# Performance work log

Hardware: AMD Instinct MI355X
Metric: run time of the kernel (lower is better)

The kernel has to match this reference:

```python
import jax, jax.numpy as jnp
import numpy as np

N_BOXES = 1_000_000
EPS = 1e-6


def box2corners(box):
    """(..., 5) [x,y,w,h,angle] -> (..., 4, 2) corners (mmcv box2corners)."""
    x, y, w, h, a = (box[..., i] for i in range(5))
    dx = jnp.asarray([0.5, -0.5, -0.5, 0.5], box.dtype) * w[..., None]  # (...,4)
    dy = jnp.asarray([0.5, 0.5, -0.5, -0.5], box.dtype) * h[..., None]
    cos, sin = jnp.cos(a)[..., None], jnp.sin(a)[..., None]
    cx = dx * cos - dy * sin + x[..., None]
    cy = dx * sin + dy * cos + y[..., None]
    return jnp.stack([cx, cy], axis=-1)


def box_intersection(c1, c2):
    """All 4x4 edge-pair segment intersections. c1,c2: (N,4,2).
    Returns pts (N,4,4,2), mask (N,4,4)."""
    roll = jnp.array([1, 2, 3, 0])
    line1 = jnp.concatenate([c1, c1[:, roll, :]], axis=-1)  # (N,4,4): x1,y1,x2,y2
    line2 = jnp.concatenate([c2, c2[:, roll, :]], axis=-1)
    l1 = line1[:, :, None, :]  # (N,4,1,4)
    l2 = line2[:, None, :, :]  # (N,1,4,4)
    x1, y1, x2, y2 = l1[..., 0], l1[..., 1], l1[..., 2], l1[..., 3]
    x3, y3, x4, y4 = l2[..., 0], l2[..., 1], l2[..., 2], l2[..., 3]
    num = (y4 - y3) * (x2 - x1) - (x4 - x3) * (y2 - y1)
    den_t = (x4 - x3) * (y1 - y3) - (y4 - y3) * (x1 - x3)
    safe = jnp.where(num == 0.0, 1.0, num)
    t = jnp.where(num == 0.0, -1.0, den_t / safe)
    mask_t = (t > 0) & (t < 1)
    den_u = (x2 - x1) * (y1 - y3) - (y2 - y1) * (x1 - x3)
    u = jnp.where(num == 0.0, -1.0, -den_u / safe)
    mask_u = (u > 0) & (u < 1)
    mask = mask_t & mask_u
    t2 = den_t / (num + 1e-8)
    pts = jnp.stack([x1 + t2 * (x2 - x1), y1 + t2 * (y2 - y1)], axis=-1)
    pts = pts * mask[..., None].astype(pts.dtype)
    return pts, mask


def box1_in_box2(c1, c2):
    """Which corners of c1 lie inside box c2. (N,4,2)x(N,4,2)->(N,4) bool."""
    a = c2[:, 0:1, :]
    b = c2[:, 1:2, :]
    d = c2[:, 3:4, :]
    ab, ad, am = b - a, d - a, c1 - a
    pab = jnp.sum(ab * am, -1) / jnp.sum(ab * ab, -1)
    pad_ = jnp.sum(ad * am, -1) / jnp.sum(ad * ad, -1)
    e = 1e-6
    return (pab > -e) & (pab < 1 + e) & (pad_ > -e) & (pad_ < 1 + e)


def intersection_area(c1, c2):
    """Differentiable rotated-box intersection area via convex polygon clipping."""
    inter_pts, inter_mask = box_intersection(c1, c2)
    m1 = box1_in_box2(c1, c2)
    m2 = box1_in_box2(c2, c1)
    n = c1.shape[0]
    verts = jnp.concatenate([c1, c2, inter_pts.reshape(n, 16, 2)], axis=1)  # (N,24,2)
    mask = jnp.concatenate([m1, m2, inter_mask.reshape(n, 16)], axis=1)     # (N,24)
    k = jnp.sum(mask, axis=-1)  # num valid vertices per box
    mf = mask.astype(verts.dtype)
    mean = jnp.sum(verts * mf[..., None], axis=1, keepdims=True) / \
        jnp.maximum(k, 1).astype(verts.dtype)[:, None, None]
    vn = verts - mean
    # sort valid vertices counterclockwise by angle around centroid; invalid last
    ang = jnp.where(mask, jnp.arctan2(vn[..., 1], vn[..., 0]), 1e9)
    order = jnp.argsort(ang, axis=-1)
    vs = jnp.take_along_axis(verts, order[..., None], axis=1)  # (N,24,2)
    idx = jnp.arange(24)
    nxt = jnp.where(idx[None, :] + 1 < k[:, None], idx[None, :] + 1, 0)
    v_next = jnp.take_along_axis(vs, nxt[..., None], axis=1)
    cross = vs[..., 0] * v_next[..., 1] - vs[..., 1] * v_next[..., 0]
    valid = idx[None, :] < k[:, None]
    return jnp.abs(jnp.sum(jnp.where(valid, cross, 0.0), axis=-1)) * 0.5


def fpdiou_loss(pred, target):
    c1 = box2corners(pred)
    c2 = box2corners(target)
    inter = intersection_area(c1, c2)
    area1 = pred[:, 2] * pred[:, 3]
    area2 = target[:, 2] * target[:, 3]
    iou = inter / (area1 + area2 - inter)
    iou = jnp.maximum(iou, EPS)
    # corner-distance term (detached in original via .detach().cpu().numpy())
    p = jax.lax.stop_gradient(c1)
    g = jax.lax.stop_gradient(c2)
    ps = jnp.take_along_axis(p, jnp.argsort(p[..., 0], axis=-1)[..., None], axis=1)
    gs = jnp.take_along_axis(g, jnp.argsort(g[..., 0], axis=-1)[..., None], axis=1)
    d = 2.0 * (gs[:, 0, 0] - ps[:, 0, 0]) ** 2 \
        + (ps[:, 1, 0] - gs[:, 1, 0]) ** 2 + (ps[:, 1, 1] - gs[:, 1, 1]) ** 2 \
        + (ps[:, 2, 0] - gs[:, 2, 0]) ** 2 + (ps[:, 2, 1] - gs[:, 2, 1]) ** 2 \
        + (ps[:, 3, 0] - gs[:, 3, 0]) ** 2 + (ps[:, 3, 1] - gs[:, 3, 1]) ** 2
    res = d / (4.0 * 1024.0 ** 2)
    loss = 1.0 - iou + res  # mode='linear'
    return jnp.mean(loss)   # reduction='mean', loss_weight=1.0


def setup_inputs() -> dict:
    key = jax.random.key(0)
    k1, k2, k3, k4 = jax.random.split(key, 4)
    xy = jax.random.uniform(k1, (N_BOXES, 2), minval=0.0, maxval=1024.0)
    wh = jax.random.uniform(k2, (N_BOXES, 2), minval=8.0, maxval=96.0)
    ang = jax.random.uniform(k3, (N_BOXES, 1), minval=-np.pi / 2, maxval=np.pi / 2)
    pred = jnp.concatenate([xy, wh, ang], axis=-1).astype(jnp.float32)
    scale = jnp.asarray([4.0, 4.0, 3.0, 3.0, 0.1], jnp.float32)
    target = pred + jax.random.normal(k4, (N_BOXES, 5), jnp.float32) * scale
    target = target.at[:, 2:4].set(jnp.maximum(target[:, 2:4], 4.0))
    return {"pred": pred, "target": target}


def reference(pred, target):
    return fpdiou_loss(pred, target)
```

## Files before the change

kernel.cpp:

```cpp
#include <hip/hip_runtime.h>

#define BS 128
#define NV 24

__device__ __forceinline__ void sort4_by_x(const float* x, const float* y,
                                           float* sx, float* sy) {
    int rk[4];
#pragma unroll
    for (int a = 0; a < 4; a++) {
        int r = 0;
#pragma unroll
        for (int b = 0; b < 4; b++) {
            r += (x[b] < x[a]) || (x[b] == x[a] && b < a);
        }
        rk[a] = r;
    }
#pragma unroll
    for (int r = 0; r < 4; r++) {
        float vx = 0.f, vy = 0.f;
#pragma unroll
        for (int a = 0; a < 4; a++) {
            if (rk[a] == r) { vx = x[a]; vy = y[a]; }
        }
        sx[r] = vx; sy[r] = vy;
    }
}

__global__ __launch_bounds__(BS, 2)
void fpdiou_kernel(const float* __restrict__ pred, const float* __restrict__ tgt,
                   float* __restrict__ partial, int n)
{
    __shared__ float s_vx[NV * BS];
    __shared__ float s_vy[NV * BS];
    __shared__ float s_ang[NV * BS];
    __shared__ float s_red[2];

    const int tid = threadIdx.x;
    const int i = blockIdx.x * BS + tid;
    float loss = 0.f;

    if (i < n) {
        const float* pp = pred + (size_t)i * 5;
        const float* gg = tgt  + (size_t)i * 5;
        const float pw = pp[2], ph = pp[3];
        const float gw = gg[2], gh = gg[3];

        float c1x[4], c1y[4], c2x[4], c2y[4];
        {
            const float DX[4] = {0.5f, -0.5f, -0.5f, 0.5f};
            const float DY[4] = {0.5f,  0.5f, -0.5f, -0.5f};
            float s, c;
            sincosf(pp[4], &s, &c);
            float x = pp[0], y = pp[1];
#pragma unroll
            for (int q = 0; q < 4; q++) {
                float dx = DX[q] * pw, dy = DY[q] * ph;
                c1x[q] = dx * c - dy * s + x;
                c1y[q] = dx * s + dy * c + y;
            }
            sincosf(gg[4], &s, &c);
            x = gg[0]; y = gg[1];
#pragma unroll
            for (int q = 0; q < 4; q++) {
                float dx = DX[q] * gw, dy = DY[q] * gh;
                c2x[q] = dx * c - dy * s + x;
                c2y[q] = dx * s + dy * c + y;
            }
        }

        int k = 0;
        {
            const float ax = c2x[0], ay = c2y[0];
            const float abx = c2x[1] - ax, aby = c2y[1] - ay;
            const float adx = c2x[3] - ax, ady = c2y[3] - ay;
            const float dab = abx * abx + aby * aby;
            const float dad = adx * adx + ady * ady;
#pragma unroll
            for (int q = 0; q < 4; q++) {
                float amx = c1x[q] - ax, amy = c1y[q] - ay;
                float pab = (abx * amx + aby * amy) / dab;
                float pd  = (adx * amx + ady * amy) / dad;
                const float e = 1e-6f;
                if (pab > -e && pab < 1.f + e && pd > -e && pd < 1.f + e) {
                    s_vx[k * BS + tid] = c1x[q];
                    s_vy[k * BS + tid] = c1y[q];
                    k++;
                }
            }
        }
        {
            const float ax = c1x[0], ay = c1y[0];
            const float abx = c1x[1] - ax, aby = c1y[1] - ay;
            const float adx = c1x[3] - ax, ady = c1y[3] - ay;
            const float dab = abx * abx + aby * aby;
            const float dad = adx * adx + ady * ady;
#pragma unroll
            for (int q = 0; q < 4; q++) {
                float amx = c2x[q] - ax, amy = c2y[q] - ay;
                float pab = (abx * amx + aby * amy) / dab;
                float pd  = (adx * amx + ady * amy) / dad;
                const float e = 1e-6f;
                if (pab > -e && pab < 1.f + e && pd > -e && pd < 1.f + e) {
                    s_vx[k * BS + tid] = c2x[q];
                    s_vy[k * BS + tid] = c2y[q];
                    k++;
                }
            }
        }
#pragma unroll
        for (int a = 0; a < 4; a++) {
            const float x1 = c1x[a], y1 = c1y[a];
            const float x2 = c1x[(a + 1) & 3], y2 = c1y[(a + 1) & 3];
            const float ex = x2 - x1, ey = y2 - y1;
#pragma unroll
            for (int b = 0; b < 4; b++) {
                const float x3 = c2x[b], y3 = c2y[b];
                const float x4 = c2x[(b + 1) & 3], y4 = c2y[(b + 1) & 3];
                const float fx = x4 - x3, fy = y4 - y3;
                const float num = fy * ex - fx * ey;
                if (num != 0.f) {
                    const float dx13 = x1 - x3, dy13 = y1 - y3;
                    const float den_t = fx * dy13 - fy * dx13;
                    const float t = den_t / num;
                    const float den_u = ex * dy13 - ey * dx13;
                    const float u = -den_u / num;
                    if (t > 0.f && t < 1.f && u > 0.f && u < 1.f) {
                        const float t2 = den_t / (num + 1e-8f);
                        s_vx[k * BS + tid] = x1 + t2 * ex;
                        s_vy[k * BS + tid] = y1 + t2 * ey;
                        k++;
                    }
                }
            }
        }

        float area = 0.f;
        if (k > 0) {
            float sx = 0.f, sy = 0.f;
            for (int v = 0; v < k; v++) {
                sx += s_vx[v * BS + tid];
                sy += s_vy[v * BS + tid];
            }
            const float mx = sx / (float)k;
            const float my = sy / (float)k;
            for (int v = 0; v < k; v++) {
                s_ang[v * BS + tid] =
                    atan2f(s_vy[v * BS + tid] - my, s_vx[v * BS + tid] - mx);
            }
            for (int v = 1; v < k; v++) {
                float a = s_ang[v * BS + tid];
                float x = s_vx[v * BS + tid];
                float y = s_vy[v * BS + tid];
                int j = v - 1;
                while (j >= 0 && s_ang[j * BS + tid] > a) {
                    s_ang[(j + 1) * BS + tid] = s_ang[j * BS + tid];
                    s_vx[(j + 1) * BS + tid] = s_vx[j * BS + tid];
                    s_vy[(j + 1) * BS + tid] = s_vy[j * BS + tid];
                    j--;
                }
                s_ang[(j + 1) * BS + tid] = a;
                s_vx[(j + 1) * BS + tid] = x;
                s_vy[(j + 1) * BS + tid] = y;
            }
            float cr = 0.f;
            for (int v = 0; v < k; v++) {
                int nx = (v + 1 < k) ? v + 1 : 0;
                cr += s_vx[v * BS + tid] * s_vy[nx * BS + tid]
                    - s_vy[v * BS + tid] * s_vx[nx * BS + tid];
            }
            area = fabsf(cr) * 0.5f;
        }

        const float a1 = pw * ph, a2 = gw * gh;
        float iou = area / (a1 + a2 - area);
        iou = fmaxf(iou, 1e-6f);

        float psx[4], psy[4], gsx[4], gsy[4];
        sort4_by_x(c1x, c1y, psx, psy);
        sort4_by_x(c2x, c2y, gsx, gsy);
        const float d0 = gsx[0] - psx[0];
        float d = 2.f * d0 * d0;
#pragma unroll
        for (int q = 1; q < 4; q++) {
            float dxq = psx[q] - gsx[q];
            float dyq = psy[q] - gsy[q];
            d += dxq * dxq + dyq * dyq;
        }
        const float res = d * (1.f / 4194304.f);

        loss = 1.f - iou + res;
    }

#pragma unroll
    for (int off = 32; off > 0; off >>= 1)
        loss += __shfl_down(loss, off, 64);
    if ((tid & 63) == 0) s_red[tid >> 6] = loss;
    __syncthreads();
    if (tid == 0) partial[blockIdx.x] = s_red[0] + s_red[1];
}

__global__ void fpdiou_reduce_kernel(const float* __restrict__ partial, int nblk,
                                     float* __restrict__ out, float inv_n)
{
    __shared__ float red[4];
    float s = 0.f;
    for (int i = threadIdx.x; i < nblk; i += blockDim.x)
        s += partial[i];
#pragma unroll
    for (int off = 32; off > 0; off >>= 1)
        s += __shfl_down(s, off, 64);
    if ((threadIdx.x & 63) == 0) red[threadIdx.x >> 6] = s;
    __syncthreads();
    if (threadIdx.x == 0) {
        float t = red[0] + red[1] + red[2] + red[3];
        out[0] = t * inv_n;
    }
}

extern "C" void kernel_launch(void* const* d_in, const int* in_sizes, int n_in,
                              void* d_out, int out_size, void* d_ws, size_t ws_size,
                              hipStream_t stream)
{
    const float* pred = (const float*)d_in[0];
    const float* tgt  = (const float*)d_in[1];
    float* out = (float*)d_out;
    const int n = in_sizes[0] / 5;
    const int nblk = (n + BS - 1) / BS;
    float* partial = (float*)d_ws;

    fpdiou_kernel<<<nblk, BS, 0, stream>>>(pred, tgt, partial, n);
    fpdiou_reduce_kernel<<<1, 256, 0, stream>>>(partial, nblk, out, 1.f / (float)n);
}
```

Baseline: 155.2 us.

## Replace atan2 sort with pseudo-angle successor search and single-wave blocks

Replaces atan2f plus insertion sort of polygon vertices with a cheap pseudo-angle and a per-vertex successor search that computes the shoelace area without sorting. Accumulates the centroid while vertices are collected, drops the num!=0 branch, caps vertex count at 16, and shrinks shared arrays. Uses 64-thread blocks so the block reduction needs no barrier, and widens the final reduce kernel to 1024 threads. The O(k^2) successor search and the unguarded division when num is zero (relying on NaN comparisons failing) change numerics slightly and add quadratic work for large k.

```diff
diff --git a/kernel.cpp b/kernel.cpp
--- a/kernel.cpp
+++ b/kernel.cpp
@@ -1,7 +1,7 @@
 #include <hip/hip_runtime.h>
 
-#define BS 128
-#define NV 24
+#define BS 64
+#define NVMAX 16
 
 __device__ __forceinline__ void sort4_by_x(const float* x, const float* y,
                                            float* sx, float* sy) {
@@ -24,16 +24,21 @@
         }
         sx[r] = vx; sy[r] = vy;
     }
+}
+
+__device__ __forceinline__ float pseudo_angle(float dx, float dy) {
+    float s = fabsf(dx) + fabsf(dy);
+    float r = (s == 0.f) ? 0.f : (1.f - dx / s);
+    return copysignf(r, dy);
 }
 
 __global__ __launch_bounds__(BS, 2)
 void fpdiou_kernel(const float* __restrict__ pred, const float* __restrict__ tgt,
                    float* __restrict__ partial, int n)
 {
-    __shared__ float s_vx[NV * BS];
-    __shared__ float s_vy[NV * BS];
-    __shared__ float s_ang[NV * BS];
-    __shared__ float s_red[2];
+    __shared__ float s_vx[NVMAX * BS];
+    __shared__ float s_vy[NVMAX * BS];
+    __shared__ float s_p [NVMAX * BS];
 
     const int tid = threadIdx.x;
     const int i = blockIdx.x * BS + tid;
@@ -69,6 +74,7 @@
         }
 
         int k = 0;
+        float sx = 0.f, sy = 0.f;
         {
             const float ax = c2x[0], ay = c2y[0];
             const float abx = c2x[1] - ax, aby = c2y[1] - ay;
@@ -84,6 +90,7 @@
                 if (pab > -e && pab < 1.f + e && pd > -e && pd < 1.f + e) {
                     s_vx[k * BS + tid] = c1x[q];
                     s_vy[k * BS + tid] = c1y[q];
+                    sx += c1x[q]; sy += c1y[q];
                     k++;
                 }
             }
@@ -103,6 +110,7 @@
                 if (pab > -e && pab < 1.f + e && pd > -e && pd < 1.f + e) {
                     s_vx[k * BS + tid] = c2x[q];
                     s_vy[k * BS + tid] = c2y[q];
+                    sx += c2x[q]; sy += c2y[q];
                     k++;
                 }
             }
@@ -110,63 +118,55 @@
 #pragma unroll
         for (int a = 0; a < 4; a++) {
             const float x1 = c1x[a], y1 = c1y[a];
-            const float x2 = c1x[(a + 1) & 3], y2 = c1y[(a + 1) & 3];
-            const float ex = x2 - x1, ey = y2 - y1;
+            const float ex = c1x[(a + 1) & 3] - x1, ey = c1y[(a + 1) & 3] - y1;
 #pragma unroll
             for (int b = 0; b < 4; b++) {
                 const float x3 = c2x[b], y3 = c2y[b];
-                const float x4 = c2x[(b + 1) & 3], y4 = c2y[(b + 1) & 3];
-                const float fx = x4 - x3, fy = y4 - y3;
+                const float fx = c2x[(b + 1) & 3] - x3, fy = c2y[(b + 1) & 3] - y3;
                 const float num = fy * ex - fx * ey;
-                if (num != 0.f) {
-                    const float dx13 = x1 - x3, dy13 = y1 - y3;
-                    const float den_t = fx * dy13 - fy * dx13;
-                    const float t = den_t / num;
-                    const float den_u = ex * dy13 - ey * dx13;
-                    const float u = -den_u / num;
-                    if (t > 0.f && t < 1.f && u > 0.f && u < 1.f) {
-                        const float t2 = den_t / (num + 1e-8f);
-                        s_vx[k * BS + tid] = x1 + t2 * ex;
-                        s_vy[k * BS + tid] = y1 + t2 * ey;
-                        k++;
-                    }
+                const float dx13 = x1 - x3, dy13 = y1 - y3;
+                const float den_t = fx * dy13 - fy * dx13;
+                const float den_u = ex * dy13 - ey * dx13;
+                const float t = den_t / num;
+                const float u = -den_u / num;
+                if (t > 0.f && t < 1.f && u > 0.f && u < 1.f && k < NVMAX) {
+                    const float t2 = den_t / (num + 1e-8f);
+                    const float ix = x1 + t2 * ex, iy = y1 + t2 * ey;
+                    s_vx[k * BS + tid] = ix;
+                    s_vy[k * BS + tid] = iy;
+                    sx += ix; sy += iy;
+                    k++;
                 }
             }
         }
 
         float area = 0.f;
         if (k > 0) {
-            float sx = 0.f, sy = 0.f;
-            for (int v = 0; v < k; v++) {
-                sx += s_vx[v * BS + tid];
-                sy += s_vy[v * BS + tid];
-            }
             const float mx = sx / (float)k;
             const float my = sy / (float)k;
             for (int v = 0; v < k; v++) {
-                s_ang[v * BS + tid] =
-                    atan2f(s_vy[v * BS + tid] - my, s_vx[v * BS + tid] - mx);
-            }
-            for (int v = 1; v < k; v++) {
-                float a = s_ang[v * BS + tid];
-                float x = s_vx[v * BS + tid];
-                float y = s_vy[v * BS + tid];
-                int j = v - 1;
-                while (j >= 0 && s_ang[j * BS + tid] > a) {
-                    s_ang[(j + 1) * BS + tid] = s_ang[j * BS + tid];
-                    s_vx[(j + 1) * BS + tid] = s_vx[j * BS + tid];
-                    s_vy[(j + 1) * BS + tid] = s_vy[j * BS + tid];
-                    j--;
-                }
-                s_ang[(j + 1) * BS + tid] = a;
-                s_vx[(j + 1) * BS + tid] = x;
-                s_vy[(j + 1) * BS + tid] = y;
+                s_p[v * BS + tid] = pseudo_angle(s_vx[v * BS + tid] - mx,
+                                                 s_vy[v * BS + tid] - my);
+            }
+            int mj = 0;
+            float mp = s_p[tid];
+            for (int j = 1; j < k; j++) {
+                float pj = s_p[j * BS + tid];
+                if (pj < mp) { mp = pj; mj = j; }
             }
             float cr = 0.f;
             for (int v = 0; v < k; v++) {
-                int nx = (v + 1 < k) ? v + 1 : 0;
-                cr += s_vx[v * BS + tid] * s_vy[nx * BS + tid]
-                    - s_vy[v * BS + tid] * s_vx[nx * BS + tid];
+                const float pv = s_p[v * BS + tid];
+                float bp = 3.4e38f;
+                int bj = -1;
+                for (int j = 0; j < k; j++) {
+                    float pj = s_p[j * BS + tid];
+                    bool gt = (pj > pv) || ((pj == pv) && (j > v));
+                    if (gt && pj < bp) { bp = pj; bj = j; }
+                }
+                const int sj = (bj >= 0) ? bj : mj;
+                cr += s_vx[v * BS + tid] * s_vy[sj * BS + tid]
+                    - s_vy[v * BS + tid] * s_vx[sj * BS + tid];
             }
             area = fabsf(cr) * 0.5f;
         }
@@ -194,15 +194,14 @@
 #pragma unroll
     for (int off = 32; off > 0; off >>= 1)
         loss += __shfl_down(loss, off, 64);
-    if ((tid & 63) == 0) s_red[tid >> 6] = loss;
-    __syncthreads();
-    if (tid == 0) partial[blockIdx.x] = s_red[0] + s_red[1];
-}
-
-__global__ void fpdiou_reduce_kernel(const float* __restrict__ partial, int nblk,
-                                     float* __restrict__ out, float inv_n)
+    if (tid == 0) partial[blockIdx.x] = loss;
+}
+
+__global__ __launch_bounds__(1024)
+void fpdiou_reduce_kernel(const float* __restrict__ partial, int nblk,
+                          float* __restrict__ out, float inv_n)
 {
-    __shared__ float red[4];
+    __shared__ float red[16];
     float s = 0.f;
     for (int i = threadIdx.x; i < nblk; i += blockDim.x)
         s += partial[i];
@@ -212,7 +211,9 @@
     if ((threadIdx.x & 63) == 0) red[threadIdx.x >> 6] = s;
     __syncthreads();
     if (threadIdx.x == 0) {
-        float t = red[0] + red[1] + red[2] + red[3];
+        float t = 0.f;
+#pragma unroll
+        for (int w = 0; w < 16; w++) t += red[w];
         out[0] = t * inv_n;
     }
 }
@@ -229,5 +230,5 @@
     float* partial = (float*)d_ws;
 
     fpdiou_kernel<<<nblk, BS, 0, stream>>>(pred, tgt, partial, n);
-    fpdiou_reduce_kernel<<<1, 256, 0, stream>>>(partial, nblk, out, 1.f / (float)n);
-}
+    fpdiou_reduce_kernel<<<1, 1024, 0, stream>>>(partial, nblk, out, 1.f / (float)n);
+}
```

Measured after the change: 152.7 us. Within noise of the previous version (-1.6%).
